# Performance work log

Hardware: AMD Instinct MI355X
Metric: run time of the kernel (lower is better)

Reference implementation:

```python
import jax, jax.numpy as jnp
import numpy as np

B, S, D = 2, 2048, 2048
H, HKV, DH = 16, 4, 128   # query heads, kv heads, head dim
N_REP = H // HKV
ROPE_BASE = 10000.0


def rotate_half(x):
    x1, x2 = x[..., : DH // 2], x[..., DH // 2 :]
    return jnp.concatenate((-x2, x1), axis=-1)


def rope_tables(seq_len, dtype=jnp.float32):
    inv_freq = 1.0 / (ROPE_BASE ** (jnp.arange(0, DH, 2, dtype=jnp.float32) / DH))
    t = jnp.arange(seq_len, dtype=jnp.float32)
    freqs = jnp.outer(t, inv_freq)                 # [S, DH/2]
    emb = jnp.concatenate((freqs, freqs), axis=-1)  # [S, DH]
    return jnp.cos(emb).astype(dtype), jnp.sin(emb).astype(dtype)


def setup_inputs() -> dict:
    key = jax.random.key(0)
    k1, k2, k3, k4, k5 = jax.random.split(key, 5)
    scale = 1.0 / np.sqrt(D)
    return {
        "hidden_states": jax.random.normal(k1, (B, S, D), dtype=jnp.float32),
        "position_ids": jnp.tile(jnp.arange(S, dtype=jnp.int32)[None, :], (B, 1)),
        "wq": jax.random.normal(k2, (D, H * DH), dtype=jnp.float32) * scale,
        "wk": jax.random.normal(k3, (D, HKV * DH), dtype=jnp.float32) * scale,
        "wv": jax.random.normal(k4, (D, HKV * DH), dtype=jnp.float32) * scale,
        "wo": jax.random.normal(k5, (H * DH, D), dtype=jnp.float32) * scale,
    }


def reference(hidden_states, position_ids, wq, wk, wv, wo):
    x = hidden_states
    b, s, _ = x.shape

    # QKV projections -> [B, H(kv), S, DH]
    q = (x @ wq).reshape(b, s, H, DH).transpose(0, 2, 1, 3)
    k = (x @ wk).reshape(b, s, HKV, DH).transpose(0, 2, 1, 3)
    v = (x @ wv).reshape(b, s, HKV, DH).transpose(0, 2, 1, 3)

    # Rotary position embedding
    cos_t, sin_t = rope_tables(s, x.dtype)
    cos = cos_t[position_ids][:, None, :, :]  # [B,1,S,DH]
    sin = sin_t[position_ids][:, None, :, :]
    q = q * cos + rotate_half(q) * sin
    k = k * cos + rotate_half(k) * sin

    # GQA: repeat KV heads to match query heads
    k = jnp.repeat(k, N_REP, axis=1)  # [B,H,S,DH]
    v = jnp.repeat(v, N_REP, axis=1)

    # Causal SDPA
    scores = jnp.einsum("bhqd,bhkd->bhqk", q, k) / jnp.sqrt(
        jnp.asarray(DH, x.dtype)
    )
    causal = jnp.tril(jnp.ones((s, s), dtype=bool))
    scores = jnp.where(causal[None, None], scores, jnp.asarray(-1e9, x.dtype))
    attn = jax.nn.softmax(scores, axis=-1)
    out = jnp.einsum("bhqk,bhkd->bhqd", attn, v)  # [B,H,S,DH]

    out = out.transpose(0, 2, 1, 3).reshape(b, s, H * DH)
    return out @ wo
```

## Files before the change

kernel.cpp:

```cpp
#include <hip/hip_runtime.h>
#include <cmath>

typedef unsigned short u16;
typedef float floatx4 __attribute__((ext_vector_type(4)));
typedef short short8 __attribute__((ext_vector_type(8)));
typedef __bf16 bf16x8 __attribute__((ext_vector_type(8)));

#define GLOBAL_AS __attribute__((address_space(1)))
#define LDS_AS __attribute__((address_space(3)))

#define S_LEN 2048
#define D_MODEL 2048
#define NH 16
#define NKV 4
#define DHEAD 128
#define SM_SCALE 0.08838834764831843f
#define K2 (SM_SCALE * 1.4426950408889634f)

__device__ __forceinline__ u16 f2bf(float f) {
    unsigned int u = __builtin_bit_cast(unsigned int, f);
    u += 0x7fffu + ((u >> 16) & 1u);
    return (u16)(u >> 16);
}
__device__ __forceinline__ u16 f2bfr(float f) {
    unsigned int u = __builtin_bit_cast(unsigned int, f);
    return (u16)((u + 0x8000u) >> 16);
}
__device__ __forceinline__ float bf2f(u16 x) {
    unsigned int u = ((unsigned int)x) << 16;
    return __builtin_bit_cast(float, u);
}
__device__ __forceinline__ floatx4 zf4() {
    floatx4 z; z[0] = 0.f; z[1] = 0.f; z[2] = 0.f; z[3] = 0.f; return z;
}
__device__ __forceinline__ floatx4 mfma16(short8 a, short8 b, floatx4 c) {
    return __builtin_amdgcn_mfma_f32_16x16x32_bf16(
        __builtin_bit_cast(bf16x8, a), __builtin_bit_cast(bf16x8, b), c, 0, 0, 0);
}
__device__ __forceinline__ void async16(const u16* g, u16* l) {
    __builtin_amdgcn_global_load_lds((GLOBAL_AS void*)g, (LDS_AS void*)l, 16, 0, 0);
}

__global__ void cast_x_kernel(const float4* __restrict__ in, ushort4* __restrict__ out) {
    int i = blockIdx.x * 256 + threadIdx.x;
    float4 v = in[i];
    ushort4 o;
    o.x = f2bf(v.x); o.y = f2bf(v.y); o.z = f2bf(v.z); o.w = f2bf(v.w);
    out[i] = o;
}

__global__ void transpose_cast_kernel(const float* __restrict__ in, u16* __restrict__ out,
                                      int R, int C) {
    __shared__ float tile[32][33];
    int tx = threadIdx.x & 31, ty = threadIdx.x >> 5;
    int bx = blockIdx.x * 32;
    int by = blockIdx.y * 32;
#pragma unroll
    for (int i = 0; i < 32; i += 8)
        tile[ty + i][tx] = in[(size_t)(by + ty + i) * C + bx + tx];
    __syncthreads();
#pragma unroll
    for (int i = 0; i < 32; i += 8)
        out[(size_t)(bx + ty + i) * R + by + tx] = f2bf(tile[tx][ty + i]);
}

__global__ void rope_tables_kernel(float* __restrict__ cs_tab, float* __restrict__ sn_tab) {
    int idx = blockIdx.x * 256 + threadIdx.x;
    int p = idx >> 6, j = idx & 63;
    double e = (double)(2 * j) / 128.0;
    double invf = pow(10000.0, -e);
    float arg = (float)p * (float)invf;
    cs_tab[idx] = (float)cos((double)arg);
    sn_tab[idx] = (float)sin((double)arg);
}

__global__ void rope_apply_kernel(u16* __restrict__ Qb, u16* __restrict__ Kb,
                                  const int* __restrict__ pos,
                                  const float4* __restrict__ cs_tab,
                                  const float4* __restrict__ sn_tab) {
    int idx = blockIdx.x * 256 + threadIdx.x;
    int j4 = idx & 15;
    int s = (idx >> 4) & 2047;
    int r = idx >> 15;
    int hh = r % 20, b = r / 20;
    int p = pos[b * S_LEN + s];
    float4 cs = cs_tab[p * 16 + j4];
    float4 sn = sn_tab[p * 16 + j4];
    u16* base;
    if (hh < 16) base = Qb + (((size_t)(b * NH + hh)) * S_LEN + s) * DHEAD;
    else         base = Kb + (((size_t)(b * NKV + (hh - 16))) * S_LEN + s) * DHEAD;
    base += j4 * 4;
    ushort4 a = *(const ushort4*)(base);
    ushort4 c = *(const ushort4*)(base + 64);
    ushort4 oa, oc;
    float x1, x2;
    x1 = bf2f(a.x); x2 = bf2f(c.x); oa.x = f2bf(x1 * cs.x - x2 * sn.x); oc.x = f2bf(x2 * cs.x + x1 * sn.x);
    x1 = bf2f(a.y); x2 = bf2f(c.y); oa.y = f2bf(x1 * cs.y - x2 * sn.y); oc.y = f2bf(x2 * cs.y + x1 * sn.y);
    x1 = bf2f(a.z); x2 = bf2f(c.z); oa.z = f2bf(x1 * cs.z - x2 * sn.z); oc.z = f2bf(x2 * cs.z + x1 * sn.z);
    x1 = bf2f(a.w); x2 = bf2f(c.w); oa.w = f2bf(x1 * cs.w - x2 * sn.w); oc.w = f2bf(x2 * cs.w + x1 * sn.w);
    *(ushort4*)(base) = oa;
    *(ushort4*)(base + 64) = oc;
}

__device__ __forceinline__ void gemm_mainloop(const u16* __restrict__ A,
                                              const u16* __restrict__ Bt,
                                              int K, u16* ldsA, u16* ldsB,
                                              floatx4 acc[4][4]) {
    const int t = threadIdx.x;
    const int lane = t & 63, wave = t >> 6;
    const int wr = wave >> 1, wc = wave & 1;
    const int lr = lane & 15, q = lane >> 4;
    const int m0 = blockIdx.y * 128, n0 = blockIdx.x * 128;
    const int swz = q ^ ((lr >> 1) & 3);

#pragma unroll
    for (int r = 0; r < 4; ++r)
#pragma unroll
        for (int c = 0; c < 4; ++c) acc[r][c] = zf4();

    for (int k0 = 0; k0 < K; k0 += 32) {
#pragma unroll
        for (int i = 0; i < 2; ++i) {
            int ci = i * 256 + t;
            int row = ci >> 2;
            int kc = ((ci & 3) ^ ((ci >> 3) & 3)) << 3;
            async16(A + (size_t)(m0 + row) * K + k0 + kc, ldsA + (i * 256 + wave * 64) * 8);
            async16(Bt + (size_t)(n0 + row) * K + k0 + kc, ldsB + (i * 256 + wave * 64) * 8);
        }
        __syncthreads();
        short8 af[4], bfr[4];
#pragma unroll
        for (int r = 0; r < 4; ++r)
            af[r] = *(const short8*)(ldsA + (wr * 64 + r * 16 + lr) * 32 + swz * 8);
#pragma unroll
        for (int c = 0; c < 4; ++c)
            bfr[c] = *(const short8*)(ldsB + (wc * 64 + c * 16 + lr) * 32 + swz * 8);
#pragma unroll
        for (int r = 0; r < 4; ++r)
#pragma unroll
            for (int c = 0; c < 4; ++c)
                acc[r][c] = mfma16(af[r], bfr[c], acc[r][c]);
        __syncthreads();
    }
}

__global__ void qkv_gemm_kernel(const u16* __restrict__ A, const u16* __restrict__ Bt,
                                u16* __restrict__ Qb, u16* __restrict__ Kb,
                                u16* __restrict__ Vt) {
    __shared__ u16 ldsA[128 * 32];
    __shared__ u16 ldsB[128 * 32];
    floatx4 acc[4][4];
    gemm_mainloop(A, Bt, D_MODEL, ldsA, ldsB, acc);

    const int t = threadIdx.x, lane = t & 63, wave = t >> 6;
    const int wr = wave >> 1, wc = wave & 1, lr = lane & 15, q = lane >> 4;
    const int m0 = blockIdx.y * 128 + wr * 64, n0 = blockIdx.x * 128 + wc * 64;
#pragma unroll
    for (int r = 0; r < 4; ++r)
#pragma unroll
        for (int c = 0; c < 4; ++c) {
            int gc = n0 + c * 16 + lr;
#pragma unroll
            for (int rr = 0; rr < 4; ++rr) {
                int grow = m0 + r * 16 + q * 4 + rr;
                int bb = grow >> 11, s = grow & 2047;
                u16 bv = f2bf(acc[r][c][rr]);
                int d = gc & 127;
                if (gc < 2048) {
                    int hh = gc >> 7;
                    Qb[(((size_t)(bb * NH + hh)) * S_LEN + s) * DHEAD + d] = bv;
                } else if (gc < 2560) {
                    int hh = (gc - 2048) >> 7;
                    Kb[(((size_t)(bb * NKV + hh)) * S_LEN + s) * DHEAD + d] = bv;
                } else {
                    int hh = (gc - 2560) >> 7;
                    Vt[(((size_t)(bb * NKV + hh)) * DHEAD + d) * S_LEN + s] = bv;
                }
            }
        }
}

__global__ void out_gemm_kernel(const u16* __restrict__ A, const u16* __restrict__ Bt,
                                float* __restrict__ out) {
    __shared__ u16 ldsA[128 * 32];
    __shared__ u16 ldsB[128 * 32];
    floatx4 acc[4][4];
    gemm_mainloop(A, Bt, D_MODEL, ldsA, ldsB, acc);

    const int t = threadIdx.x, lane = t & 63, wave = t >> 6;
    const int wr = wave >> 1, wc = wave & 1, lr = lane & 15, q = lane >> 4;
    const int m0 = blockIdx.y * 128 + wr * 64, n0 = blockIdx.x * 128 + wc * 64;
#pragma unroll
    for (int r = 0; r < 4; ++r)
#pragma unroll
        for (int c = 0; c < 4; ++c) {
            int gc = n0 + c * 16 + lr;
#pragma unroll
            for (int rr = 0; rr < 4; ++rr) {
                int grow = m0 + r * 16 + q * 4 + rr;
                out[(size_t)grow * D_MODEL + gc] = acc[r][c][rr];
            }
        }
}

__global__ __launch_bounds__(256, 4) void fa_kernel(const u16* __restrict__ Qb,
                                                    const u16* __restrict__ Kb,
                                                    const u16* __restrict__ Vt,
                                                    u16* __restrict__ Ob) {
    __shared__ u16 ldsK[64 * 128];
    __shared__ u16 ldsV[128 * 64];
    __shared__ u16 ldsP[4 * 16 * 64];

    const int t = threadIdx.x, lane = t & 63, wave = t >> 6;
    const int lr = lane & 15, q = lane >> 4;
    const int swz = lr & 7;

    const int bid = blockIdx.x;
    const int qt = bid >> 5;
    const int bh = bid & 31;
    const int b = bh >> 4, h = bh & 15;
    const int kvh = h >> 2;

    const u16* Kp = Kb + (size_t)(b * NKV + kvh) * S_LEN * DHEAD;
    const u16* Vp = Vt + (size_t)(b * NKV + kvh) * DHEAD * S_LEN;
    const u16* Qp = Qb + ((size_t)((b * NH + h) * S_LEN) + qt * 64 + wave * 16) * DHEAD;

    short8 qf[4];
#pragma unroll
    for (int kk = 0; kk < 4; ++kk)
        qf[kk] = *(const short8*)(Qp + (size_t)lr * DHEAD + kk * 32 + q * 8);

    floatx4 accO[8];
#pragma unroll
    for (int d = 0; d < 8; ++d) accO[d] = zf4();
    float m_i[4] = {-3e38f, -3e38f, -3e38f, -3e38f};
    float l_i[4] = {0.f, 0.f, 0.f, 0.f};

    const int nkt = qt + 1;
    for (int kt = 0; kt < nkt; ++kt) {
#pragma unroll
        for (int i = 0; i < 4; ++i) {
            int ci = i * 256 + t;
            int krow = ci >> 4, kc = ((ci & 15) ^ ((ci >> 4) & 7)) << 3;
            async16(Kp + (size_t)(kt * 64 + krow) * DHEAD + kc,
                    ldsK + (i * 256 + wave * 64) * 8);
            int dh = ci >> 3, vc = ((ci & 7) ^ ((ci >> 3) & 7)) << 3;
            async16(Vp + (size_t)dh * S_LEN + kt * 64 + vc,
                    ldsV + (i * 256 + wave * 64) * 8);
        }
        __syncthreads();

        floatx4 sc[4];
#pragma unroll
        for (int c = 0; c < 4; ++c) {
            sc[c] = zf4();
#pragma unroll
            for (int kk = 0; kk < 4; ++kk) {
                short8 kb = *(const short8*)(ldsK + (c * 16 + lr) * DHEAD +
                                             (((kk * 4 + q) ^ swz) << 3));
                sc[c] = mfma16(qf[kk], kb, sc[c]);
            }
        }

        const bool diag = (kt == qt);
#pragma unroll
        for (int rr = 0; rr < 4; ++rr) {
            int ql = wave * 16 + q * 4 + rr;
            float mx = -3e38f;
#pragma unroll
            for (int c = 0; c < 4; ++c) {
                float s = sc[c][rr];
                if (diag && (c * 16 + lr) > ql) s = -3e38f;
                sc[c][rr] = s;
                mx = fmaxf(mx, s);
            }
            mx = fmaxf(mx, __shfl_xor(mx, 1));
            mx = fmaxf(mx, __shfl_xor(mx, 2));
            mx = fmaxf(mx, __shfl_xor(mx, 4));
            mx = fmaxf(mx, __shfl_xor(mx, 8));
            float mnew = fmaxf(m_i[rr], mx);
            float mk = mnew * K2;
            float alpha = __builtin_amdgcn_exp2f(fmaf(m_i[rr], K2, -mk));
            m_i[rr] = mnew;
            float rs = 0.f;
#pragma unroll
            for (int c = 0; c < 4; ++c) {
                float p = __builtin_amdgcn_exp2f(fmaf(sc[c][rr], K2, -mk));
                sc[c][rr] = p;
                rs += p;
            }
            rs += __shfl_xor(rs, 1);
            rs += __shfl_xor(rs, 2);
            rs += __shfl_xor(rs, 4);
            rs += __shfl_xor(rs, 8);
            l_i[rr] = l_i[rr] * alpha + rs;
#pragma unroll
            for (int d = 0; d < 8; ++d) accO[d][rr] *= alpha;
        }

        u16* Pw = ldsP + wave * 1024;
#pragma unroll
        for (int c = 0; c < 4; ++c)
#pragma unroll
            for (int rr = 0; rr < 4; ++rr) {
                int prow = q * 4 + rr;
                int pch = (c * 2 + (lr >> 3)) ^ (prow & 7);
                Pw[prow * 64 + pch * 8 + (lr & 7)] = f2bfr(sc[c][rr]);
            }

#pragma unroll
        for (int kk2 = 0; kk2 < 2; ++kk2) {
            short8 pa = *(const short8*)(Pw + lr * 64 + (((kk2 * 4 + q) ^ swz) << 3));
#pragma unroll
            for (int d = 0; d < 8; ++d) {
                short8 vb = *(const short8*)(ldsV + (d * 16 + lr) * 64 +
                                             (((kk2 * 4 + q) ^ swz) << 3));
                accO[d] = mfma16(pa, vb, accO[d]);
            }
        }
        __syncthreads();
    }

    const int tok0 = qt * 64 + wave * 16;
#pragma unroll
    for (int rr = 0; rr < 4; ++rr) {
        float inv = 1.0f / l_i[rr];
        size_t rowoff = ((size_t)(b * S_LEN + tok0 + q * 4 + rr)) * (NH * DHEAD) + h * DHEAD;
#pragma unroll
        for (int d = 0; d < 8; ++d)
            Ob[rowoff + d * 16 + lr] = f2bf(accO[d][rr] * inv);
    }
}

extern "C" void kernel_launch(void* const* d_in, const int* in_sizes, int n_in,
                              void* d_out, int out_size, void* d_ws, size_t ws_size,
                              hipStream_t stream) {
    const float* X  = (const float*)d_in[0];
    const int* pos  = (const int*)d_in[1];
    const float* wq = (const float*)d_in[2];
    const float* wk = (const float*)d_in[3];
    const float* wv = (const float*)d_in[4];
    const float* wo = (const float*)d_in[5];
    float* out = (float*)d_out;

    char* w = (char*)d_ws;
    u16* Xbf    = (u16*)(w);
    u16* Wqkv   = (u16*)(w + 16777216);
    u16* Wo     = (u16*)(w + 29360128);
    u16* Qb     = (u16*)(w + 37748736);
    u16* Kb     = (u16*)(w + 54525952);
    u16* Vt     = (u16*)(w + 58720256);
    u16* Ob     = (u16*)(w + 62914560);
    float* cst  = (float*)(w + 79691776);
    float* snt  = (float*)(w + 80216064);

    cast_x_kernel<<<8192, 256, 0, stream>>>((const float4*)X, (ushort4*)Xbf);
    transpose_cast_kernel<<<dim3(64, 64), 256, 0, stream>>>(wq, Wqkv, 2048, 2048);
    transpose_cast_kernel<<<dim3(16, 64), 256, 0, stream>>>(wk, Wqkv + (size_t)2048 * 2048, 2048, 512);
    transpose_cast_kernel<<<dim3(16, 64), 256, 0, stream>>>(wv, Wqkv + (size_t)2560 * 2048, 2048, 512);
    transpose_cast_kernel<<<dim3(64, 64), 256, 0, stream>>>(wo, Wo, 2048, 2048);
    rope_tables_kernel<<<512, 256, 0, stream>>>(cst, snt);
    qkv_gemm_kernel<<<dim3(24, 32), 256, 0, stream>>>(Xbf, Wqkv, Qb, Kb, Vt);
    rope_apply_kernel<<<5120, 256, 0, stream>>>(Qb, Kb, pos, (const float4*)cst, (const float4*)snt);
    fa_kernel<<<1024, 256, 0, stream>>>(Qb, Kb, Vt, Ob);
    out_gemm_kernel<<<dim3(16, 32), 256, 0, stream>>>(Ob, Wo, out);
}
```

Measured before the change: 354.4 us.

## Compute transposed S in flash attention to keep P in registers

Swaps the MFMA operands so the score tile is computed as K·Q^T, which gives each lane one query row. The row max and sum then need only two cross-lane shuffles and a single m/l scalar per lane. P is fed straight from registers into 16x16x16 bf16 MFMAs against V^T, removing the LDS round-trip for P and its scratch buffer. The kernel also launches the heaviest causal query tiles first to improve load balance, and the output stores become 4-wide vector writes. The trade-off is that the PV product now uses the smaller-K MFMA variant, which needs twice as many instructions.

```diff
diff --git a/kernel.cpp b/kernel.cpp
--- a/kernel.cpp
+++ b/kernel.cpp
@@ -4,6 +4,7 @@
 typedef unsigned short u16;
 typedef float floatx4 __attribute__((ext_vector_type(4)));
 typedef short short8 __attribute__((ext_vector_type(8)));
+typedef short short4v __attribute__((ext_vector_type(4)));
 typedef __bf16 bf16x8 __attribute__((ext_vector_type(8)));
 
 #define GLOBAL_AS __attribute__((address_space(1)))
@@ -36,6 +37,9 @@
 __device__ __forceinline__ floatx4 mfma16(short8 a, short8 b, floatx4 c) {
     return __builtin_amdgcn_mfma_f32_16x16x32_bf16(
         __builtin_bit_cast(bf16x8, a), __builtin_bit_cast(bf16x8, b), c, 0, 0, 0);
+}
+__device__ __forceinline__ floatx4 mfma16k16(short4v a, short4v b, floatx4 c) {
+    return __builtin_amdgcn_mfma_f32_16x16x16bf16_1k(a, b, c, 0, 0, 0);
 }
 __device__ __forceinline__ void async16(const u16* g, u16* l) {
     __builtin_amdgcn_global_load_lds((GLOBAL_AS void*)g, (LDS_AS void*)l, 16, 0, 0);
@@ -209,14 +213,13 @@
                                                     u16* __restrict__ Ob) {
     __shared__ u16 ldsK[64 * 128];
     __shared__ u16 ldsV[128 * 64];
-    __shared__ u16 ldsP[4 * 16 * 64];
 
     const int t = threadIdx.x, lane = t & 63, wave = t >> 6;
     const int lr = lane & 15, q = lane >> 4;
     const int swz = lr & 7;
 
     const int bid = blockIdx.x;
-    const int qt = bid >> 5;
+    const int qt = 31 - (bid >> 5);
     const int bh = bid & 31;
     const int b = bh >> 4, h = bh & 15;
     const int kvh = h >> 2;
@@ -233,8 +236,7 @@
     floatx4 accO[8];
 #pragma unroll
     for (int d = 0; d < 8; ++d) accO[d] = zf4();
-    float m_i[4] = {-3e38f, -3e38f, -3e38f, -3e38f};
-    float l_i[4] = {0.f, 0.f, 0.f, 0.f};
+    float m_i = -3e38f, l_i = 0.f;
 
     const int nkt = qt + 1;
     for (int kt = 0; kt < nkt; ++kt) {
@@ -256,79 +258,79 @@
             sc[c] = zf4();
 #pragma unroll
             for (int kk = 0; kk < 4; ++kk) {
-                short8 kb = *(const short8*)(ldsK + (c * 16 + lr) * DHEAD +
-                                             (((kk * 4 + q) ^ swz) << 3));
-                sc[c] = mfma16(qf[kk], kb, sc[c]);
-            }
-        }
-
-        const bool diag = (kt == qt);
-#pragma unroll
-        for (int rr = 0; rr < 4; ++rr) {
-            int ql = wave * 16 + q * 4 + rr;
-            float mx = -3e38f;
-#pragma unroll
-            for (int c = 0; c < 4; ++c) {
-                float s = sc[c][rr];
-                if (diag && (c * 16 + lr) > ql) s = -3e38f;
-                sc[c][rr] = s;
-                mx = fmaxf(mx, s);
-            }
-            mx = fmaxf(mx, __shfl_xor(mx, 1));
-            mx = fmaxf(mx, __shfl_xor(mx, 2));
-            mx = fmaxf(mx, __shfl_xor(mx, 4));
-            mx = fmaxf(mx, __shfl_xor(mx, 8));
-            float mnew = fmaxf(m_i[rr], mx);
-            float mk = mnew * K2;
-            float alpha = __builtin_amdgcn_exp2f(fmaf(m_i[rr], K2, -mk));
-            m_i[rr] = mnew;
-            float rs = 0.f;
-#pragma unroll
-            for (int c = 0; c < 4; ++c) {
+                short8 kfr = *(const short8*)(ldsK + (c * 16 + lr) * DHEAD +
+                                              (((kk * 4 + q) ^ swz) << 3));
+                sc[c] = mfma16(kfr, qf[kk], sc[c]);
+            }
+        }
+
+        if (kt == qt) {
+            const int qrow = wave * 16 + lr;
+#pragma unroll
+            for (int c = 0; c < 4; ++c)
+#pragma unroll
+                for (int rr = 0; rr < 4; ++rr)
+                    if (c * 16 + q * 4 + rr > qrow) sc[c][rr] = -3e38f;
+        }
+
+        float mx = -3e38f;
+#pragma unroll
+        for (int c = 0; c < 4; ++c)
+#pragma unroll
+            for (int rr = 0; rr < 4; ++rr) mx = fmaxf(mx, sc[c][rr]);
+        mx = fmaxf(mx, __shfl_xor(mx, 16));
+        mx = fmaxf(mx, __shfl_xor(mx, 32));
+        float mnew = fmaxf(m_i, mx);
+        float mk = mnew * K2;
+        float alpha = __builtin_amdgcn_exp2f(fmaf(m_i, K2, -mk));
+        m_i = mnew;
+        float rs = 0.f;
+#pragma unroll
+        for (int c = 0; c < 4; ++c)
+#pragma unroll
+            for (int rr = 0; rr < 4; ++rr) {
                 float p = __builtin_amdgcn_exp2f(fmaf(sc[c][rr], K2, -mk));
                 sc[c][rr] = p;
                 rs += p;
             }
-            rs += __shfl_xor(rs, 1);
-            rs += __shfl_xor(rs, 2);
-            rs += __shfl_xor(rs, 4);
-            rs += __shfl_xor(rs, 8);
-            l_i[rr] = l_i[rr] * alpha + rs;
-#pragma unroll
-            for (int d = 0; d < 8; ++d) accO[d][rr] *= alpha;
-        }
-
-        u16* Pw = ldsP + wave * 1024;
-#pragma unroll
-        for (int c = 0; c < 4; ++c)
-#pragma unroll
-            for (int rr = 0; rr < 4; ++rr) {
-                int prow = q * 4 + rr;
-                int pch = (c * 2 + (lr >> 3)) ^ (prow & 7);
-                Pw[prow * 64 + pch * 8 + (lr & 7)] = f2bfr(sc[c][rr]);
-            }
-
-#pragma unroll
-        for (int kk2 = 0; kk2 < 2; ++kk2) {
-            short8 pa = *(const short8*)(Pw + lr * 64 + (((kk2 * 4 + q) ^ swz) << 3));
+        rs += __shfl_xor(rs, 16);
+        rs += __shfl_xor(rs, 32);
+        l_i = l_i * alpha + rs;
+#pragma unroll
+        for (int d = 0; d < 8; ++d) accO[d] *= alpha;
+
+        short4v pb[4];
+#pragma unroll
+        for (int c = 0; c < 4; ++c) {
+            pb[c][0] = (short)f2bfr(sc[c][0]);
+            pb[c][1] = (short)f2bfr(sc[c][1]);
+            pb[c][2] = (short)f2bfr(sc[c][2]);
+            pb[c][3] = (short)f2bfr(sc[c][3]);
+        }
+
+#pragma unroll
+        for (int ks = 0; ks < 4; ++ks)
 #pragma unroll
             for (int d = 0; d < 8; ++d) {
-                short8 vb = *(const short8*)(ldsV + (d * 16 + lr) * 64 +
-                                             (((kk2 * 4 + q) ^ swz) << 3));
-                accO[d] = mfma16(pa, vb, accO[d]);
-            }
-        }
+                short4v vf = *(const short4v*)(ldsV + (d * 16 + lr) * 64 +
+                                               (((ks * 2 + (q >> 1)) ^ swz) << 3) +
+                                               (q & 1) * 4);
+                accO[d] = mfma16k16(vf, pb[ks], accO[d]);
+            }
         __syncthreads();
     }
 
-    const int tok0 = qt * 64 + wave * 16;
-#pragma unroll
-    for (int rr = 0; rr < 4; ++rr) {
-        float inv = 1.0f / l_i[rr];
-        size_t rowoff = ((size_t)(b * S_LEN + tok0 + q * 4 + rr)) * (NH * DHEAD) + h * DHEAD;
-#pragma unroll
-        for (int d = 0; d < 8; ++d)
-            Ob[rowoff + d * 16 + lr] = f2bf(accO[d][rr] * inv);
+    const int tok = qt * 64 + wave * 16 + lr;
+    const float inv = 1.0f / l_i;
+    u16* orow = Ob + ((size_t)(b * S_LEN + tok)) * (NH * DHEAD) + h * DHEAD + q * 4;
+#pragma unroll
+    for (int d = 0; d < 8; ++d) {
+        ushort4 o;
+        o.x = f2bf(accO[d][0] * inv);
+        o.y = f2bf(accO[d][1] * inv);
+        o.z = f2bf(accO[d][2] * inv);
+        o.w = f2bf(accO[d][3] * inv);
+        *(ushort4*)(orow + d * 16) = o;
     }
 }
 
```

Measured after the change: 326.3 us. -7.9%, faster.
